# Optimization experiments

Measured on AMD Instinct MI355X. Metric: run time of the kernel, lower is better.

Reference implementation:

```python
import jax, jax.numpy as jnp
import numpy as np

# Faithful translations of the torch lambdas:
# r0: identity; r90: transpose(-2,-1); r180: flip(-2); r270: transpose(-2,-1) then flip(-1)
_r0 = lambda xi: xi
_r90 = lambda xi: jnp.swapaxes(xi, -2, -1)
_r180 = lambda xi: jnp.flip(xi, axis=-2)
_r270 = lambda xi: jnp.flip(jnp.swapaxes(xi, -2, -1), axis=-1)


def setup_inputs() -> dict:
    key = jax.random.key(0)
    kx, kl = jax.random.split(key)
    B, C, H, W = 256, 3, 224, 224  # square spatial required by transpose-in-place semantics
    x = jax.random.normal(kx, (B, C, H, W), dtype=jnp.float32)
    label = jax.random.randint(kl, (B,), 0, 4, dtype=jnp.int32)
    return {"x": x, "label": label}


def reference(x, label):
    # Single fused per-sample-indexed rotation via vmap + lax.switch —
    # replaces the python loop / per-sample kernel launches of the original.
    def rotate_one(xi, li):
        return jax.lax.switch(li, [_r0, _r90, _r180, _r270], xi)

    out = jax.vmap(rotate_one)(x, label)
    return (out, label)
```

## Files before the change

### kernel.cpp

```cpp
#include <hip/hip_runtime.h>


#define HW 224
#define TILE 32
#define NT 7

__global__ __launch_bounds__(256) void rot4_kernel(const float* __restrict__ x,
                                                   const int* __restrict__ label,
                                                   float* __restrict__ out) {
    int tile = blockIdx.x;
    int tw = tile % NT; tile /= NT;
    int th = tile % NT; tile /= NT;
    int c  = tile % 3;  tile /= 3;
    int b  = tile;

    const int lab = label[b];
    const size_t plane = (size_t)(b * 3 + c) * (HW * HW);
    const float* __restrict__ in = x + plane;
    float* __restrict__ o = out + plane;

    const int h0 = th * TILE;
    const int w0 = tw * TILE;

    const int t  = threadIdx.x;
    const int r  = t >> 3;
    const int c4 = t & 7;

    if (lab == 0 || lab == 2) {
        const int in_row = (lab == 0) ? (h0 + r) : (HW - 1 - (h0 + r));
        float4 v = *(const float4*)(in + (size_t)in_row * HW + w0 + c4 * 4);
        *(float4*)(o + (size_t)(h0 + r) * HW + w0 + c4 * 4) = v;
    } else {
        __shared__ float tb[TILE][TILE + 1];
        const int rbase = (lab == 1) ? w0 : (HW - TILE - w0);
        float4 v = *(const float4*)(in + (size_t)(rbase + r) * HW + h0 + c4 * 4);
        tb[r][c4 * 4 + 0] = v.x;
        tb[r][c4 * 4 + 1] = v.y;
        tb[r][c4 * 4 + 2] = v.z;
        tb[r][c4 * 4 + 3] = v.w;
        __syncthreads();
        float4 w;
        if (lab == 1) {
            w.x = tb[c4 * 4 + 0][r];
            w.y = tb[c4 * 4 + 1][r];
            w.z = tb[c4 * 4 + 2][r];
            w.w = tb[c4 * 4 + 3][r];
        } else {
            w.x = tb[31 - (c4 * 4 + 0)][r];
            w.y = tb[31 - (c4 * 4 + 1)][r];
            w.z = tb[31 - (c4 * 4 + 2)][r];
            w.w = tb[31 - (c4 * 4 + 3)][r];
        }
        *(float4*)(o + (size_t)(h0 + r) * HW + w0 + c4 * 4) = w;
    }
}

__global__ void label_kernel(const int* __restrict__ label, float* __restrict__ out, int n) {
    int i = blockIdx.x * blockDim.x + threadIdx.x;
    if (i < n) out[i] = (float)label[i];
}

extern "C" void kernel_launch(void* const* d_in, const int* in_sizes, int n_in,
                              void* d_out, int out_size, void* d_ws, size_t ws_size,
                              hipStream_t stream) {
    const float* x     = (const float*)d_in[0];
    const int*   label = (const int*)d_in[1];
    float*       out   = (float*)d_out;

    const int B = in_sizes[1];
    const int nblocks = B * 3 * NT * NT;

    rot4_kernel<<<nblocks, 256, 0, stream>>>(x, label, out);

    const size_t img_elems = (size_t)B * 3 * HW * HW;
    label_kernel<<<(B + 255) / 256, 256, 0, stream>>>(label, out + img_elems, B);
}
```

Baseline: 261.9 us.

## Process full 32-row bands per block and fold label copy into main kernel

Each block now handles a 32-row band of one plane, a 7x coarser unit than the previous single 32x32 tile. Loads and stores are unrolled 7 times, and the transpose cases stage seven tiles in shared memory behind one barrier. The separate label-conversion kernel is removed and its work is done by one extra block, saving a launch. The cost is more shared memory per block (about 30KB) and fewer blocks, which may lower occupancy. The label block assumes B <= 256.

```diff
diff --git a/kernel.cpp b/kernel.cpp
--- a/kernel.cpp
+++ b/kernel.cpp
@@ -1,63 +1,78 @@
 #include <hip/hip_runtime.h>
 
 
-#define HW 224
+#define HW   224
 #define TILE 32
-#define NT 7
+#define NT   7
+#define ROW4 56
 
-__global__ __launch_bounds__(256) void rot4_kernel(const float* __restrict__ x,
-                                                   const int* __restrict__ label,
-                                                   float* __restrict__ out) {
-    int tile = blockIdx.x;
-    int tw = tile % NT; tile /= NT;
-    int th = tile % NT; tile /= NT;
-    int c  = tile % 3;  tile /= 3;
-    int b  = tile;
+__global__ __launch_bounds__(256) void rot4_band(const float* __restrict__ x,
+                                                 const int* __restrict__ label,
+                                                 float* __restrict__ out,
+                                                 int nimg_blocks, int B) {
+    const int i = blockIdx.x;
+    const int t = threadIdx.x;
+
+    if (i >= nimg_blocks) {
+        const size_t img_elems = (size_t)B * 3 * HW * HW;
+        if (t < B) out[img_elems + t] = (float)label[t];
+        return;
+    }
+
+    int tmp = i;
+    const int band = tmp % NT; tmp /= NT;
+    const int c    = tmp % 3;  tmp /= 3;
+    const int b    = tmp;
 
     const int lab = label[b];
     const size_t plane = (size_t)(b * 3 + c) * (HW * HW);
     const float* __restrict__ in = x + plane;
     float* __restrict__ o = out + plane;
 
-    const int h0 = th * TILE;
-    const int w0 = tw * TILE;
-
-    const int t  = threadIdx.x;
-    const int r  = t >> 3;
-    const int c4 = t & 7;
+    const int h0 = band * TILE;
 
     if (lab == 0 || lab == 2) {
-        const int in_row = (lab == 0) ? (h0 + r) : (HW - 1 - (h0 + r));
-        float4 v = *(const float4*)(in + (size_t)in_row * HW + w0 + c4 * 4);
-        *(float4*)(o + (size_t)(h0 + r) * HW + w0 + c4 * 4) = v;
+#pragma unroll
+        for (int k = 0; k < NT; ++k) {
+            const int idx = k * 256 + t;
+            const int r   = idx / ROW4;
+            const int c4  = idx % ROW4;
+            const int orow = h0 + r;
+            const int irow = (lab == 0) ? orow : (HW - 1 - orow);
+            float4 v = *(const float4*)(in + (size_t)irow * HW + c4 * 4);
+            *(float4*)(o + (size_t)orow * HW + c4 * 4) = v;
+        }
     } else {
-        __shared__ float tb[TILE][TILE + 1];
-        const int rbase = (lab == 1) ? w0 : (HW - TILE - w0);
-        float4 v = *(const float4*)(in + (size_t)(rbase + r) * HW + h0 + c4 * 4);
-        tb[r][c4 * 4 + 0] = v.x;
-        tb[r][c4 * 4 + 1] = v.y;
-        tb[r][c4 * 4 + 2] = v.z;
-        tb[r][c4 * 4 + 3] = v.w;
+        __shared__ float tb[NT][TILE][TILE + 1];
+        const int wl = t >> 3;
+        const int c4 = t & 7;
+#pragma unroll
+        for (int k = 0; k < NT; ++k) {
+            const int rbase = (lab == 1) ? k * TILE : (HW - TILE - k * TILE);
+            float4 v = *(const float4*)(in + (size_t)(rbase + wl) * HW + h0 + c4 * 4);
+            tb[k][wl][c4 * 4 + 0] = v.x;
+            tb[k][wl][c4 * 4 + 1] = v.y;
+            tb[k][wl][c4 * 4 + 2] = v.z;
+            tb[k][wl][c4 * 4 + 3] = v.w;
+        }
         __syncthreads();
-        float4 w;
-        if (lab == 1) {
-            w.x = tb[c4 * 4 + 0][r];
-            w.y = tb[c4 * 4 + 1][r];
-            w.z = tb[c4 * 4 + 2][r];
-            w.w = tb[c4 * 4 + 3][r];
-        } else {
-            w.x = tb[31 - (c4 * 4 + 0)][r];
-            w.y = tb[31 - (c4 * 4 + 1)][r];
-            w.z = tb[31 - (c4 * 4 + 2)][r];
-            w.w = tb[31 - (c4 * 4 + 3)][r];
+#pragma unroll
+        for (int k = 0; k < NT; ++k) {
+            float4 w;
+            if (lab == 1) {
+                w.x = tb[k][c4 * 4 + 0][wl];
+                w.y = tb[k][c4 * 4 + 1][wl];
+                w.z = tb[k][c4 * 4 + 2][wl];
+                w.w = tb[k][c4 * 4 + 3][wl];
+            } else {
+                w.x = tb[k][31 - (c4 * 4 + 0)][wl];
+                w.y = tb[k][31 - (c4 * 4 + 1)][wl];
+                w.z = tb[k][31 - (c4 * 4 + 2)][wl];
+                w.w = tb[k][31 - (c4 * 4 + 3)][wl];
+            }
+            *(float4*)(o + (size_t)(h0 + wl) * HW + k * TILE + c4 * 4) = w;
         }
-        *(float4*)(o + (size_t)(h0 + r) * HW + w0 + c4 * 4) = w;
     }
-}
-
-__global__ void label_kernel(const int* __restrict__ label, float* __restrict__ out, int n) {
-    int i = blockIdx.x * blockDim.x + threadIdx.x;
-    if (i < n) out[i] = (float)label[i];
 }
 
 extern "C" void kernel_launch(void* const* d_in, const int* in_sizes, int n_in,
@@ -68,10 +83,8 @@
     float*       out   = (float*)d_out;
 
     const int B = in_sizes[1];
-    const int nblocks = B * 3 * NT * NT;
+    const int nimg_blocks = B * 3 * NT;
+    const int nblocks = nimg_blocks + 1;
 
-    rot4_kernel<<<nblocks, 256, 0, stream>>>(x, label, out);
-
-    const size_t img_elems = (size_t)B * 3 * HW * HW;
-    label_kernel<<<(B + 255) / 256, 256, 0, stream>>>(label, out + img_elems, B);
+    rot4_band<<<nblocks, 256, 0, stream>>>(x, label, out, nimg_blocks, B);
 }
```

Result: no change. 264.5 us (+1.0%).
